# Optimization experiments

Hardware: AMD Instinct MI355X
Metric: run time of the kernel (lower is better)

The kernel has to match this reference:

```python
import jax, jax.numpy as jnp
import numpy as np

VOCAB_SIZE = 62  # string.ascii_letters + string.digits
HIDDEN = 1024
STATE = int(HIDDEN * 4.0)  # state_size_mult=4.0
B, L = 2, 2048


def setup_inputs() -> dict:
    key = jax.random.key(0)
    ks = jax.random.split(key, 6)
    g = lambda k, shape, scale: (jax.random.normal(k, shape, jnp.float32) * scale)
    return {
        "tokens": jax.random.randint(ks[0], (B, L), 0, VOCAB_SIZE),
        "embed_w": g(ks[1], (VOCAB_SIZE, HIDDEN), 1.0),
        "norm_w": jnp.ones((HIDDEN,), jnp.float32),
        "in_w": g(ks[2], (HIDDEN, 4 * STATE), HIDDEN ** -0.5),
        "in_b": jnp.zeros((4 * STATE,), jnp.float32),
        "out_w": g(ks[3], (STATE, HIDDEN), STATE ** -0.5),
        "out_b": jnp.zeros((HIDDEN,), jnp.float32),
        "head_w": g(ks[4], (HIDDEN, VOCAB_SIZE), HIDDEN ** -0.5),
        "head_b": jnp.zeros((VOCAB_SIZE,), jnp.float32),
    }


def _rmsnorm(x, w, eps=1e-6):
    var = jnp.mean(x * x, axis=-1, keepdims=True)
    return x * jax.lax.rsqrt(var + eps) * w


def reference(tokens, embed_w, norm_w, in_w, in_b, out_w, out_b, head_w, head_b):
    # embedding lookup: [B, L, H]
    x = embed_w[tokens]
    res = x
    xn = _rmsnorm(x, norm_w)
    # single fused projection to (x_inner, a, b, c), each [B, L, STATE]
    proj = xn @ in_w + in_b
    xg, a_l, b_l, c_l = jnp.split(proj, 4, axis=-1)
    a = jax.nn.sigmoid(a_l)            # forget gate in (0,1)
    bx = jax.nn.sigmoid(b_l) * xg      # input contribution b_t * x_t
    # linear recurrence h_t = a_t * h_{t-1} + b_t * x_t via associative scan
    def comb(e1, e2):
        a1, h1 = e1
        a2, h2 = e2
        return a1 * a2, a2 * h1 + h2
    _, h = jax.lax.associative_scan(comb, (a, bx), axis=1)
    y = jax.nn.sigmoid(c_l) * h        # output gate c_t * h_t
    out = y @ out_w + out_b + res      # project back to hidden + residual
    return out @ head_w + head_b       # vocab logits [B, L, 62]
```

## Files before the change

kernel.cpp:

```cpp
#include <hip/hip_runtime.h>
#include <math.h>

#define HID   1024
#define STT   4096
#define MTOK  4096
#define LSEQ  2048
#define NCHUNK 64
#define CHUNK  32
#define VOCAB  62

typedef __attribute__((ext_vector_type(8))) short short8v;
typedef __attribute__((ext_vector_type(4))) float float4v;

typedef const __attribute__((address_space(1))) void* gptr_t;
typedef __attribute__((address_space(3))) void* lptr_t;

__device__ __forceinline__ float sigmoidf_(float x) {
    return 1.0f / (1.0f + __expf(-x));
}
__device__ __forceinline__ unsigned short f2bf(float f) {
    unsigned int u = __float_as_uint(f);
    unsigned int r = (u + 0x7fffu + ((u >> 16) & 1u)) >> 16;
    return (unsigned short)r;
}
__device__ __forceinline__ float bf2f(unsigned short b) {
    return __uint_as_float(((unsigned int)b) << 16);
}

__global__ __launch_bounds__(256) void cast_transpose_kernel(
    const float* __restrict__ src, unsigned short* __restrict__ dst, int R, int C)
{
    __shared__ float tile[32][33];
    int c0 = blockIdx.x * 32, r0 = blockIdx.y * 32;
    int t = threadIdx.x;
    int r = t >> 3, c4 = (t & 7) << 2;
    float4 v = *(const float4*)(src + (size_t)(r0 + r) * C + c0 + c4);
    tile[r][c4 + 0] = v.x; tile[r][c4 + 1] = v.y;
    tile[r][c4 + 2] = v.z; tile[r][c4 + 3] = v.w;
    __syncthreads();
    int oc = t >> 3;
    int orr = (t & 7) << 2;
    ushort4 o;
    o.x = f2bf(tile[orr + 0][oc]); o.y = f2bf(tile[orr + 1][oc]);
    o.z = f2bf(tile[orr + 2][oc]); o.w = f2bf(tile[orr + 3][oc]);
    *(ushort4*)(dst + (size_t)(c0 + oc) * R + r0 + orr) = o;
}

__global__ __launch_bounds__(256) void embed_norm_kernel(
    const int* __restrict__ tokens, const float* __restrict__ embed_w,
    const float* __restrict__ norm_w, unsigned short* __restrict__ xn)
{
    int m = blockIdx.x;
    int t = threadIdx.x;
    int tok = tokens[m];
    float4 x = ((const float4*)(embed_w + (size_t)tok * HID))[t];
    float ss = x.x * x.x + x.y * x.y + x.z * x.z + x.w * x.w;
    for (int off = 32; off > 0; off >>= 1) ss += __shfl_down(ss, off);
    __shared__ float wsum[4];
    if ((t & 63) == 0) wsum[t >> 6] = ss;
    __syncthreads();
    float tot = wsum[0] + wsum[1] + wsum[2] + wsum[3];
    float scale = rsqrtf(tot / (float)HID + 1e-6f);
    float4 w4 = ((const float4*)norm_w)[t];
    ushort4 o;
    o.x = f2bf(x.x * scale * w4.x); o.y = f2bf(x.y * scale * w4.y);
    o.z = f2bf(x.z * scale * w4.z); o.w = f2bf(x.w * scale * w4.w);
    *(ushort4*)(xn + (size_t)m * HID + (t << 2)) = o;
}

__global__ __launch_bounds__(256) void w2t_kernel(
    const float* __restrict__ out_w, const float* __restrict__ head_w,
    unsigned short* __restrict__ W2T)
{
    __shared__ float red[4][4][64];
    int tid = threadIdx.x;
    int jc = tid >> 6, n = tid & 63;
    int k0 = blockIdx.x * 4;
    bool act = n < VOCAB;
    float a[4] = {0.f, 0.f, 0.f, 0.f};
    int j0 = jc * 256;
    const float* w0 = out_w + (size_t)(k0 + 0) * HID;
    const float* w1 = out_w + (size_t)(k0 + 1) * HID;
    const float* w2 = out_w + (size_t)(k0 + 2) * HID;
    const float* w3 = out_w + (size_t)(k0 + 3) * HID;
    #pragma unroll 4
    for (int j = j0; j < j0 + 256; j++) {
        float h = act ? head_w[(size_t)j * VOCAB + n] : 0.f;
        a[0] = fmaf(w0[j], h, a[0]);
        a[1] = fmaf(w1[j], h, a[1]);
        a[2] = fmaf(w2[j], h, a[2]);
        a[3] = fmaf(w3[j], h, a[3]);
    }
    #pragma unroll
    for (int i = 0; i < 4; i++) red[jc][i][n] = a[i];
    __syncthreads();
    if (jc == 0) {
        #pragma unroll
        for (int i = 0; i < 4; i++) {
            float s = red[0][i][n] + red[1][i][n] + red[2][i][n] + red[3][i][n];
            W2T[(size_t)n * STT + k0 + i] = f2bf(s);
        }
    }
}

__global__ __launch_bounds__(256) void ehead_kernel(
    const float* __restrict__ embed_w, const float* __restrict__ out_b,
    const float* __restrict__ head_w, const float* __restrict__ head_b,
    float* __restrict__ E_head)
{
    __shared__ float part[4][64];
    int t = blockIdx.x;
    int n = threadIdx.x & 63, jc = threadIdx.x >> 6;
    const float* src = (t < VOCAB) ? (embed_w + (size_t)t * HID) : out_b;
    float acc = 0.f;
    if (n < VOCAB) {
        int j0 = jc * 256;
        #pragma unroll 4
        for (int j = j0; j < j0 + 256; j++)
            acc = fmaf(src[j], head_w[(size_t)j * VOCAB + n], acc);
    }
    part[jc][n] = acc;
    __syncthreads();
    if (threadIdx.x < 64) {
        float s = part[0][n] + part[1][n] + part[2][n] + part[3][n];
        if (t == VOCAB && n < VOCAB) s += head_b[n];
        E_head[t * 64 + n] = s;
    }
}

__global__ __launch_bounds__(512, 2) void gemm_in_mfma(
    const unsigned short* __restrict__ A, const unsigned short* __restrict__ B,
    const float* __restrict__ bias,
    unsigned short* __restrict__ a_out, unsigned short* __restrict__ bx_out,
    unsigned short* __restrict__ c_out)
{
    extern __shared__ unsigned short lds[];
    int tid = threadIdx.x;
    int wid = tid >> 6, lane = tid & 63;
    int wg = blockIdx.x;
    int xcd = wg & 7, loc = wg >> 3;
    int by = ((xcd >> 1) << 2) + (loc & 3);
    int bx = ((xcd & 1) << 5) + (loc >> 2);
    int m0 = by * 256, s0 = bx * 64;
    int wm = wid >> 2, wn = wid & 3;
    int lr = lane & 15, lk = lane >> 4;

    int cb0 = wid * 64, cb1 = 512 + wid * 64;
    int p0 = cb0 + lane, p1 = cb1 + lane;
    int row0 = p0 >> 2, ks0 = (p0 & 3) ^ ((row0 >> 1) & 3);
    int row1 = p1 >> 2, ks1 = (p1 & 3) ^ ((row1 >> 1) & 3);
    int arow0 = m0 + row0, arow1 = m0 + row1;
    int brow0 = ((row0 >> 6) << 12) + s0 + (row0 & 63);
    int brow1 = ((row1 >> 6) << 12) + s0 + (row1 & 63);

#define SHALF(grow0, grow1, b, which, kt, kk) do {                               \
    unsigned short* _d = lds + (b) * 32768 + (which) * 16384 + (kk) * 8192;      \
    __builtin_amdgcn_global_load_lds(                                            \
        (gptr_t)(const void*)(((which) ? B : A) + (size_t)(grow0) * 1024 +       \
                              (kt) * 64 + (kk) * 32 + ks0 * 8),                  \
        (lptr_t)(void*)(_d + (size_t)cb0 * 8), 16, 0, 0);                        \
    __builtin_amdgcn_global_load_lds(                                            \
        (gptr_t)(const void*)(((which) ? B : A) + (size_t)(grow1) * 1024 +       \
                              (kt) * 64 + (kk) * 32 + ks1 * 8),                  \
        (lptr_t)(void*)(_d + (size_t)cb1 * 8), 16, 0, 0);                        \
} while (0)

    int ksw = lk ^ ((lr >> 1) & 3);

#define RD_A(b, kk, mf) \
    (*(const short8v*)&lds[(b) * 32768 + (kk) * 8192 + \
        (((wm * 128 + (mf) * 16 + lr) << 2) + ksw) * 8])
#define RD_B(b, kk, nf) \
    (*(const short8v*)&lds[(b) * 32768 + 16384 + (kk) * 8192 + \
        ((((nf) * 64 + wn * 16 + lr) << 2) + ksw) * 8])

#define MFMA8x2(AF, B0, B1, n0i, n1i) do {                                       \
    __builtin_amdgcn_s_setprio(1);                                               \
    _Pragma("unroll")                                                            \
    for (int mf = 0; mf < 8; mf++) {                                             \
        acc[mf][n0i] = __builtin_amdgcn_mfma_f32_16x16x32_bf16(                  \
            (AF)[mf], (B0), acc[mf][n0i], 0, 0, 0);                              \
        acc[mf][n1i] = __builtin_amdgcn_mfma_f32_16x16x32_bf16(                  \
            (AF)[mf], (B1), acc[mf][n1i], 0, 0, 0);                              \
    }                                                                            \
    __builtin_amdgcn_s_setprio(0);                                               \
} while (0)

#define BAR_IN()  do { __builtin_amdgcn_s_barrier();                              \
    asm volatile("s_waitcnt lgkmcnt(0)" ::: "memory");                           \
    __builtin_amdgcn_sched_barrier(0); } while (0)
#define BAR_OUT() do { asm volatile("" ::: "memory");                             \
    __builtin_amdgcn_s_barrier(); } while (0)

    float4v acc[8][4];
    float4v z = {0.f, 0.f, 0.f, 0.f};
    #pragma unroll
    for (int i = 0; i < 8; i++)
        #pragma unroll
        for (int j = 0; j < 4; j++) acc[i][j] = z;

    SHALF(arow0, arow1, 0, 0, 0, 0); SHALF(brow0, brow1, 0, 1, 0, 0);
    SHALF(arow0, arow1, 0, 0, 0, 1); SHALF(brow0, brow1, 0, 1, 0, 1);
    asm volatile("s_waitcnt vmcnt(0)" ::: "memory");
    __builtin_amdgcn_s_barrier();

    short8v af[8], bf0, bf1;

    for (int kt = 0; kt < 16; ++kt) {
        int cur = kt & 1, nxt = cur ^ 1;
        int ktn = kt < 15 ? kt + 1 : 15;
        #pragma unroll
        for (int mf = 0; mf < 8; mf++) af[mf] = RD_A(cur, 0, mf);
        bf0 = RD_B(cur, 0, 0); bf1 = RD_B(cur, 0, 1);
        asm volatile("s_waitcnt vmcnt(4)" ::: "memory");
        SHALF(arow0, arow1, nxt, 0, ktn, 0);
        BAR_IN();
        MFMA8x2(af, bf0, bf1, 0, 1);
        BAR_OUT();
        bf0 = RD_B(cur, 0, 2); bf1 = RD_B(cur, 0, 3);
        SHALF(brow0, brow1, nxt, 1, ktn, 0);
        BAR_IN();
        MFMA8x2(af, bf0, bf1, 2, 3);
        BAR_OUT();
        #pragma unroll
        for (int mf = 0; mf < 8; mf++) af[mf] = RD_A(cur, 1, mf);
        bf0 = RD_B(cur, 1, 0); bf1 = RD_B(cur, 1, 1);
        asm volatile("s_waitcnt vmcnt(4)" ::: "memory");
        SHALF(arow0, arow1, nxt, 0, ktn, 1);
        BAR_IN();
        MFMA8x2(af, bf0, bf1, 0, 1);
        BAR_OUT();
        bf0 = RD_B(cur, 1, 2); bf1 = RD_B(cur, 1, 3);
        SHALF(brow0, brow1, nxt, 1, ktn, 1);
        BAR_IN();
        MFMA8x2(af, bf0, bf1, 2, 3);
        BAR_OUT();
    }

    int s = s0 + wn * 16 + lr;
    float b_xg = bias[s];
    float b_a  = bias[4096 + s];
    float b_b  = bias[8192 + s];
    float b_c  = bias[12288 + s];
    int rbase = lk << 2;
    #pragma unroll
    for (int mf = 0; mf < 8; mf++)
        #pragma unroll
        for (int q = 0; q < 4; q++) {
            int m = m0 + wm * 128 + mf * 16 + rbase + q;
            size_t idx = (size_t)m * STT + s;
            float xg = acc[mf][0][q] + b_xg;
            float a  = sigmoidf_(acc[mf][1][q] + b_a);
            float bxv = sigmoidf_(acc[mf][2][q] + b_b) * xg;
            float c  = sigmoidf_(acc[mf][3][q] + b_c);
            a_out[idx]  = f2bf(a);
            bx_out[idx] = f2bf(bxv);
            c_out[idx]  = f2bf(c);
        }
#undef SHALF
#undef RD_A
#undef RD_B
#undef MFMA8x2
#undef BAR_IN
#undef BAR_OUT
}

__global__ __launch_bounds__(256, 3) void logits_gemm(
    const unsigned short* __restrict__ Y, const unsigned short* __restrict__ W2T,
    float* __restrict__ part)
{
    extern __shared__ unsigned short lds[];
    int tid = threadIdx.x;
    int wid = tid >> 6, lane = tid & 63;
    int wg = blockIdx.x;
    int m0 = (wg & 31) * 128;
    int slice = wg >> 5;
    int ks0 = slice * 512;
    int wm = wid >> 1, wn = wid & 1;
    int lr = lane & 15, lk = lane >> 4;

    auto stage = [&](int b, int kt) {
        unsigned short* As = lds + b * 6144;
        unsigned short* Bs = As + 4096;
        #pragma unroll
        for (int i = 0; i < 2; i++) {
            int cb = i * 256 + wid * 64;
            int p = cb + lane;
            int row = p >> 2;
            int ks = (p & 3) ^ ((row >> 1) & 3);
            __builtin_amdgcn_global_load_lds(
                (gptr_t)(const void*)(Y + (size_t)(m0 + row) * STT + kt + ks * 8),
                (lptr_t)(void*)(As + (size_t)cb * 8), 16, 0, 0);
        }
        {
            int cb = wid * 64;
            int p = cb + lane;
            int row = p >> 2;
            int ks = (p & 3) ^ ((row >> 1) & 3);
            __builtin_amdgcn_global_load_lds(
                (gptr_t)(const void*)(W2T + (size_t)row * STT + kt + ks * 8),
                (lptr_t)(void*)(Bs + (size_t)cb * 8), 16, 0, 0);
        }
    };

    float4v acc[4][2];
    float4v z = {0.f, 0.f, 0.f, 0.f};
    #pragma unroll
    for (int i = 0; i < 4; i++) { acc[i][0] = z; acc[i][1] = z; }

    const int nt = 16;
    stage(0, ks0); stage(1, ks0 + 32);

    int ksw = lk ^ ((lr >> 1) & 3);

    for (int t = 0; t < nt; ++t) {
        if (t + 2 < nt) stage((t + 2) % 3, ks0 + (t + 2) * 32);
        if (t + 2 < nt)      asm volatile("s_waitcnt vmcnt(6)" ::: "memory");
        else if (t + 1 < nt) asm volatile("s_waitcnt vmcnt(3)" ::: "memory");
        else                 asm volatile("s_waitcnt vmcnt(0)" ::: "memory");
        __builtin_amdgcn_s_barrier();
        asm volatile("" ::: "memory");
        const unsigned short* As = lds + (t % 3) * 6144;
        const unsigned short* Bs = As + 4096;
        short8v af[4], bfr[2];
        #pragma unroll
        for (int f = 0; f < 4; f++)
            af[f] = *(const short8v*)&As[(((wm * 64 + f * 16 + lr) << 2) + ksw) * 8];
        #pragma unroll
        for (int g = 0; g < 2; g++)
            bfr[g] = *(const short8v*)&Bs[(((wn * 32 + g * 16 + lr) << 2) + ksw) * 8];
        __builtin_amdgcn_s_setprio(1);
        #pragma unroll
        for (int f = 0; f < 4; f++)
            #pragma unroll
            for (int g = 0; g < 2; g++)
                acc[f][g] = __builtin_amdgcn_mfma_f32_16x16x32_bf16(
                    af[f], bfr[g], acc[f][g], 0, 0, 0);
        __builtin_amdgcn_s_setprio(0);
        asm volatile("" ::: "memory");
        __builtin_amdgcn_s_barrier();
    }

    float* pb = part + (size_t)slice * MTOK * 64;
    int rbase = lk << 2;
    #pragma unroll
    for (int f = 0; f < 4; f++)
        #pragma unroll
        for (int g = 0; g < 2; g++) {
            int n = wn * 32 + g * 16 + lr;
            #pragma unroll
            for (int q = 0; q < 4; q++) {
                int m = m0 + wm * 64 + f * 16 + rbase + q;
                pb[(size_t)m * 64 + n] = acc[f][g][q];
            }
        }
}

__global__ __launch_bounds__(64) void logits_reduce(
    const float* __restrict__ part, const float* __restrict__ E_head,
    const int* __restrict__ tokens, float* __restrict__ logits)
{
    int m = blockIdx.x;
    int n = threadIdx.x;
    if (n >= VOCAB) return;
    int tok = tokens[m];
    float s = E_head[tok * 64 + n] + E_head[VOCAB * 64 + n];
    #pragma unroll
    for (int sl = 0; sl < 8; sl++)
        s += part[(size_t)sl * MTOK * 64 + (size_t)m * 64 + n];
    logits[(size_t)m * VOCAB + n] = s;
}

__global__ __launch_bounds__(256) void scan_phase1(
    const unsigned short* __restrict__ a_buf, const unsigned short* __restrict__ bx_buf,
    float* __restrict__ chunkA, float* __restrict__ chunkH)
{
    int bid = blockIdx.x;
    int sg = bid & 3, q = (bid >> 2) & 63, b = bid >> 8;
    int s0 = sg * 1024 + threadIdx.x * 4;
    size_t base = (size_t)(b * LSEQ + q * CHUNK) * STT + s0;
    const unsigned short* ap = a_buf + base;
    const unsigned short* bp = bx_buf + base;
    float Aa[4] = {1.f, 1.f, 1.f, 1.f}, Hh[4] = {0.f, 0.f, 0.f, 0.f};
    for (int t = 0; t < CHUNK; t++) {
        ushort4 Av = *(const ushort4*)ap;
        ushort4 Bv = *(const ushort4*)bp;
        const unsigned short* avp = (const unsigned short*)&Av;
        const unsigned short* bvp = (const unsigned short*)&Bv;
        #pragma unroll
        for (int j = 0; j < 4; j++) {
            float a = bf2f(avp[j]);
            Hh[j] = fmaf(a, Hh[j], bf2f(bvp[j]));
            Aa[j] *= a;
        }
        ap += STT; bp += STT;
    }
    #pragma unroll
    for (int j = 0; j < 4; j++) {
        int ch = b * STT + s0 + j;
        chunkA[ch * NCHUNK + q] = Aa[j];
        chunkH[ch * NCHUNK + q] = Hh[j];
    }
}

__global__ __launch_bounds__(256) void scan_phase2(
    const float* __restrict__ chunkA, const float* __restrict__ chunkH,
    float* __restrict__ carry)
{
    int ch = blockIdx.x * 256 + threadIdx.x;
    float c = 0.f;
    for (int q = 0; q < NCHUNK; q++) {
        carry[ch * NCHUNK + q] = c;
        c = fmaf(chunkA[ch * NCHUNK + q], c, chunkH[ch * NCHUNK + q]);
    }
}

__global__ __launch_bounds__(256) void scan_phase3(
    const unsigned short* __restrict__ a_buf, const unsigned short* __restrict__ bx_buf,
    const unsigned short* __restrict__ c_buf, const float* __restrict__ carry,
    unsigned short* __restrict__ y)
{
    int bid = blockIdx.x;
    int sg = bid & 3, q = (bid >> 2) & 63, b = bid >> 8;
    int s0 = sg * 1024 + threadIdx.x * 4;
    float h[4];
    #pragma unroll
    for (int j = 0; j < 4; j++)
        h[j] = carry[(b * STT + s0 + j) * NCHUNK + q];
    size_t base = (size_t)(b * LSEQ + q * CHUNK) * STT + s0;
    const unsigned short* ap = a_buf + base;
    const unsigned short* bp = bx_buf + base;
    const unsigned short* cp = c_buf + base;
    unsigned short* yp = y + base;
    for (int t = 0; t < CHUNK; t++) {
        ushort4 Av = *(const ushort4*)ap;
        ushort4 Bv = *(const ushort4*)bp;
        ushort4 Cv = *(const ushort4*)cp;
        const unsigned short* avp = (const unsigned short*)&Av;
        const unsigned short* bvp = (const unsigned short*)&Bv;
        const unsigned short* cvp = (const unsigned short*)&Cv;
        ushort4 o;
        unsigned short* op = (unsigned short*)&o;
        #pragma unroll
        for (int j = 0; j < 4; j++) {
            h[j] = fmaf(bf2f(avp[j]), h[j], bf2f(bvp[j]));
            op[j] = f2bf(bf2f(cvp[j]) * h[j]);
        }
        *(ushort4*)yp = o;
        ap += STT; bp += STT; cp += STT; yp += STT;
    }
}

extern "C" void kernel_launch(void* const* d_in, const int* in_sizes, int n_in,
                              void* d_out, int out_size, void* d_ws, size_t ws_size,
                              hipStream_t stream) {
    const int*   tokens  = (const int*)d_in[0];
    const float* embed_w = (const float*)d_in[1];
    const float* norm_w  = (const float*)d_in[2];
    const float* in_w    = (const float*)d_in[3];
    const float* in_b    = (const float*)d_in[4];
    const float* out_w   = (const float*)d_in[5];
    const float* out_b   = (const float*)d_in[6];
    const float* head_w  = (const float*)d_in[7];
    const float* head_b  = (const float*)d_in[8];
    float* logits = (float*)d_out;

    char* w = (char*)d_ws;
    unsigned short* a_buf  = (unsigned short*)w;
    unsigned short* bx_buf = (unsigned short*)(w + 33554432);
    unsigned short* c_buf  = (unsigned short*)(w + 67108864);
    unsigned short* W2T    = (unsigned short*)(w + 100663296);
    float*          E_head = (float*)(w + 101711872);
    float*          part   = (float*)(w + 102760448);
    unsigned short* y      = (unsigned short*)(w + 134217728);
    unsigned short* in_wT  = (unsigned short*)(w + 167772160);
    unsigned short* xn     = (unsigned short*)(w + 201326592);
    float* chunkA = (float*)(w + 209715200);
    float* chunkH = chunkA + 8192 * NCHUNK;
    float* carry  = chunkH + 8192 * NCHUNK;

    hipLaunchKernelGGL(cast_transpose_kernel, dim3(16384 / 32, 1024 / 32), dim3(256), 0, stream,
                       in_w, in_wT, 1024, 16384);
    hipLaunchKernelGGL(embed_norm_kernel, dim3(MTOK), dim3(256), 0, stream,
                       tokens, embed_w, norm_w, xn);
    hipLaunchKernelGGL(w2t_kernel, dim3(1024), dim3(256), 0, stream,
                       out_w, head_w, W2T);
    hipLaunchKernelGGL(ehead_kernel, dim3(VOCAB + 1), dim3(256), 0, stream,
                       embed_w, out_b, head_w, head_b, E_head);
    hipLaunchKernelGGL(gemm_in_mfma, dim3(1024), dim3(512), 131072, stream,
                       xn, in_wT, in_b, a_buf, bx_buf, c_buf);
    hipLaunchKernelGGL(scan_phase1, dim3(512), dim3(256), 0, stream,
                       a_buf, bx_buf, chunkA, chunkH);
    hipLaunchKernelGGL(scan_phase2, dim3(32), dim3(256), 0, stream,
                       chunkA, chunkH, carry);
    hipLaunchKernelGGL(scan_phase3, dim3(512), dim3(256), 0, stream,
                       a_buf, bx_buf, c_buf, carry, y);
    hipLaunchKernelGGL(logits_gemm, dim3(256), dim3(256), 36864, stream,
                       y, W2T, part);
    hipLaunchKernelGGL(logits_reduce, dim3(MTOK), dim3(64), 0, stream,
                       part, E_head, tokens, logits);
}
```

Baseline: 291.2 us.

## Shrink input GEMM tiles to single-buffered 128x128 blocks and merge prep kernels

The fused input projection GEMM moves from 256x256 output tiles with 512 threads and double-buffered 128KB LDS to 128x128 tiles (32 state columns times four gates) with 256 threads, a 16KB static LDS tile and a simple load-wait-compute loop over k-steps of 32. The aim is higher occupancy and more workgroups to spread across CUs. In exchange it gives up load/compute overlap, lowers MFMA work per LDS byte and adds a barrier every k-step. Separately, the W2T and E_head precompute kernels are merged into one launch to cut launch overhead.

```diff
diff --git a/kernel.cpp b/kernel.cpp
--- a/kernel.cpp
+++ b/kernel.cpp
@@ -68,201 +68,160 @@
     *(ushort4*)(xn + (size_t)m * HID + (t << 2)) = o;
 }
 
-__global__ __launch_bounds__(256) void w2t_kernel(
+__global__ __launch_bounds__(256) void prep_kernel(
     const float* __restrict__ out_w, const float* __restrict__ head_w,
-    unsigned short* __restrict__ W2T)
+    const float* __restrict__ embed_w, const float* __restrict__ out_b,
+    const float* __restrict__ head_b,
+    unsigned short* __restrict__ W2T, float* __restrict__ E_head)
 {
     __shared__ float red[4][4][64];
     int tid = threadIdx.x;
     int jc = tid >> 6, n = tid & 63;
-    int k0 = blockIdx.x * 4;
     bool act = n < VOCAB;
-    float a[4] = {0.f, 0.f, 0.f, 0.f};
-    int j0 = jc * 256;
-    const float* w0 = out_w + (size_t)(k0 + 0) * HID;
-    const float* w1 = out_w + (size_t)(k0 + 1) * HID;
-    const float* w2 = out_w + (size_t)(k0 + 2) * HID;
-    const float* w3 = out_w + (size_t)(k0 + 3) * HID;
-    #pragma unroll 4
-    for (int j = j0; j < j0 + 256; j++) {
-        float h = act ? head_w[(size_t)j * VOCAB + n] : 0.f;
-        a[0] = fmaf(w0[j], h, a[0]);
-        a[1] = fmaf(w1[j], h, a[1]);
-        a[2] = fmaf(w2[j], h, a[2]);
-        a[3] = fmaf(w3[j], h, a[3]);
-    }
-    #pragma unroll
-    for (int i = 0; i < 4; i++) red[jc][i][n] = a[i];
-    __syncthreads();
-    if (jc == 0) {
-        #pragma unroll
-        for (int i = 0; i < 4; i++) {
-            float s = red[0][i][n] + red[1][i][n] + red[2][i][n] + red[3][i][n];
-            W2T[(size_t)n * STT + k0 + i] = f2bf(s);
-        }
-    }
-}
-
-__global__ __launch_bounds__(256) void ehead_kernel(
-    const float* __restrict__ embed_w, const float* __restrict__ out_b,
-    const float* __restrict__ head_w, const float* __restrict__ head_b,
-    float* __restrict__ E_head)
-{
-    __shared__ float part[4][64];
-    int t = blockIdx.x;
-    int n = threadIdx.x & 63, jc = threadIdx.x >> 6;
-    const float* src = (t < VOCAB) ? (embed_w + (size_t)t * HID) : out_b;
-    float acc = 0.f;
-    if (n < VOCAB) {
+    if (blockIdx.x < 1024) {
+        int k0 = blockIdx.x * 4;
+        float a[4] = {0.f, 0.f, 0.f, 0.f};
         int j0 = jc * 256;
+        const float* w0 = out_w + (size_t)(k0 + 0) * HID;
+        const float* w1 = out_w + (size_t)(k0 + 1) * HID;
+        const float* w2 = out_w + (size_t)(k0 + 2) * HID;
+        const float* w3 = out_w + (size_t)(k0 + 3) * HID;
         #pragma unroll 4
-        for (int j = j0; j < j0 + 256; j++)
-            acc = fmaf(src[j], head_w[(size_t)j * VOCAB + n], acc);
-    }
-    part[jc][n] = acc;
-    __syncthreads();
-    if (threadIdx.x < 64) {
-        float s = part[0][n] + part[1][n] + part[2][n] + part[3][n];
-        if (t == VOCAB && n < VOCAB) s += head_b[n];
-        E_head[t * 64 + n] = s;
-    }
-}
-
-__global__ __launch_bounds__(512, 2) void gemm_in_mfma(
+        for (int j = j0; j < j0 + 256; j++) {
+            float h = act ? head_w[(size_t)j * VOCAB + n] : 0.f;
+            a[0] = fmaf(w0[j], h, a[0]);
+            a[1] = fmaf(w1[j], h, a[1]);
+            a[2] = fmaf(w2[j], h, a[2]);
+            a[3] = fmaf(w3[j], h, a[3]);
+        }
+        #pragma unroll
+        for (int i = 0; i < 4; i++) red[jc][i][n] = a[i];
+        __syncthreads();
+        if (jc == 0) {
+            #pragma unroll
+            for (int i = 0; i < 4; i++) {
+                float s = red[0][i][n] + red[1][i][n] + red[2][i][n] + red[3][i][n];
+                W2T[(size_t)n * STT + k0 + i] = f2bf(s);
+            }
+        }
+    } else {
+        int t = blockIdx.x - 1024;
+        const float* src = (t < VOCAB) ? (embed_w + (size_t)t * HID) : out_b;
+        float acc = 0.f;
+        if (act) {
+            int j0 = jc * 256;
+            #pragma unroll 4
+            for (int j = j0; j < j0 + 256; j++)
+                acc = fmaf(src[j], head_w[(size_t)j * VOCAB + n], acc);
+        }
+        red[jc][0][n] = acc;
+        __syncthreads();
+        if (tid < 64) {
+            float s = red[0][0][n] + red[1][0][n] + red[2][0][n] + red[3][0][n];
+            if (t == VOCAB && act) s += head_b[n];
+            E_head[t * 64 + n] = s;
+        }
+    }
+}
+
+__global__ __launch_bounds__(256) void gemm_in_mfma(
     const unsigned short* __restrict__ A, const unsigned short* __restrict__ B,
     const float* __restrict__ bias,
     unsigned short* __restrict__ a_out, unsigned short* __restrict__ bx_out,
     unsigned short* __restrict__ c_out)
 {
-    extern __shared__ unsigned short lds[];
+    __shared__ __align__(16) unsigned short lds[8192];
     int tid = threadIdx.x;
     int wid = tid >> 6, lane = tid & 63;
     int wg = blockIdx.x;
     int xcd = wg & 7, loc = wg >> 3;
-    int by = ((xcd >> 1) << 2) + (loc & 3);
-    int bx = ((xcd & 1) << 5) + (loc >> 2);
-    int m0 = by * 256, s0 = bx * 64;
-    int wm = wid >> 2, wn = wid & 3;
+    int by = (xcd >> 2) * 16 + (loc & 15);
+    int slab = (xcd & 3) * 32 + (loc >> 4);
+    int m0 = by * 128, s0 = slab * 32;
     int lr = lane & 15, lk = lane >> 4;
 
-    int cb0 = wid * 64, cb1 = 512 + wid * 64;
+    int cb0 = wid * 64, cb1 = 256 + wid * 64;
     int p0 = cb0 + lane, p1 = cb1 + lane;
-    int row0 = p0 >> 2, ks0 = (p0 & 3) ^ ((row0 >> 1) & 3);
-    int row1 = p1 >> 2, ks1 = (p1 & 3) ^ ((row1 >> 1) & 3);
-    int arow0 = m0 + row0, arow1 = m0 + row1;
-    int brow0 = ((row0 >> 6) << 12) + s0 + (row0 & 63);
-    int brow1 = ((row1 >> 6) << 12) + s0 + (row1 & 63);
-
-#define SHALF(grow0, grow1, b, which, kt, kk) do {                               \
-    unsigned short* _d = lds + (b) * 32768 + (which) * 16384 + (kk) * 8192;      \
+    int r0 = p0 >> 2, k0s = (p0 & 3) ^ ((r0 >> 1) & 3);
+    int r1 = p1 >> 2, k1s = (p1 & 3) ^ ((r1 >> 1) & 3);
+    int arow0 = m0 + r0, arow1 = m0 + r1;
+    int bcol0 = ((r0 >> 5) << 12) + s0 + (r0 & 31);
+    int bcol1 = ((r1 >> 5) << 12) + s0 + (r1 & 31);
+
+#define STAGE(kt) do {                                                           \
     __builtin_amdgcn_global_load_lds(                                            \
-        (gptr_t)(const void*)(((which) ? B : A) + (size_t)(grow0) * 1024 +       \
-                              (kt) * 64 + (kk) * 32 + ks0 * 8),                  \
-        (lptr_t)(void*)(_d + (size_t)cb0 * 8), 16, 0, 0);                        \
+        (gptr_t)(const void*)(A + (size_t)arow0 * 1024 + (kt) * 32 + k0s * 8),   \
+        (lptr_t)(void*)(lds + cb0 * 8), 16, 0, 0);                               \
     __builtin_amdgcn_global_load_lds(                                            \
-        (gptr_t)(const void*)(((which) ? B : A) + (size_t)(grow1) * 1024 +       \
-                              (kt) * 64 + (kk) * 32 + ks1 * 8),                  \
-        (lptr_t)(void*)(_d + (size_t)cb1 * 8), 16, 0, 0);                        \
+        (gptr_t)(const void*)(A + (size_t)arow1 * 1024 + (kt) * 32 + k1s * 8),   \
+        (lptr_t)(void*)(lds + cb1 * 8), 16, 0, 0);                               \
+    __builtin_amdgcn_global_load_lds(                                            \
+        (gptr_t)(const void*)(B + (size_t)bcol0 * 1024 + (kt) * 32 + k0s * 8),   \
+        (lptr_t)(void*)(lds + 4096 + cb0 * 8), 16, 0, 0);                        \
+    __builtin_amdgcn_global_load_lds(                                            \
+        (gptr_t)(const void*)(B + (size_t)bcol1 * 1024 + (kt) * 32 + k1s * 8),   \
+        (lptr_t)(void*)(lds + 4096 + cb1 * 8), 16, 0, 0);                        \
 } while (0)
 
     int ksw = lk ^ ((lr >> 1) & 3);
 
-#define RD_A(b, kk, mf) \
-    (*(const short8v*)&lds[(b) * 32768 + (kk) * 8192 + \
-        (((wm * 128 + (mf) * 16 + lr) << 2) + ksw) * 8])
-#define RD_B(b, kk, nf) \
-    (*(const short8v*)&lds[(b) * 32768 + 16384 + (kk) * 8192 + \
-        ((((nf) * 64 + wn * 16 + lr) << 2) + ksw) * 8])
-
-#define MFMA8x2(AF, B0, B1, n0i, n1i) do {                                       \
-    __builtin_amdgcn_s_setprio(1);                                               \
-    _Pragma("unroll")                                                            \
-    for (int mf = 0; mf < 8; mf++) {                                             \
-        acc[mf][n0i] = __builtin_amdgcn_mfma_f32_16x16x32_bf16(                  \
-            (AF)[mf], (B0), acc[mf][n0i], 0, 0, 0);                              \
-        acc[mf][n1i] = __builtin_amdgcn_mfma_f32_16x16x32_bf16(                  \
-            (AF)[mf], (B1), acc[mf][n1i], 0, 0, 0);                              \
-    }                                                                            \
-    __builtin_amdgcn_s_setprio(0);                                               \
-} while (0)
-
-#define BAR_IN()  do { __builtin_amdgcn_s_barrier();                              \
-    asm volatile("s_waitcnt lgkmcnt(0)" ::: "memory");                           \
-    __builtin_amdgcn_sched_barrier(0); } while (0)
-#define BAR_OUT() do { asm volatile("" ::: "memory");                             \
-    __builtin_amdgcn_s_barrier(); } while (0)
-
-    float4v acc[8][4];
+    float4v acc[2][8];
     float4v z = {0.f, 0.f, 0.f, 0.f};
     #pragma unroll
-    for (int i = 0; i < 8; i++)
-        #pragma unroll
-        for (int j = 0; j < 4; j++) acc[i][j] = z;
-
-    SHALF(arow0, arow1, 0, 0, 0, 0); SHALF(brow0, brow1, 0, 1, 0, 0);
-    SHALF(arow0, arow1, 0, 0, 0, 1); SHALF(brow0, brow1, 0, 1, 0, 1);
-    asm volatile("s_waitcnt vmcnt(0)" ::: "memory");
-    __builtin_amdgcn_s_barrier();
-
-    short8v af[8], bf0, bf1;
-
-    for (int kt = 0; kt < 16; ++kt) {
-        int cur = kt & 1, nxt = cur ^ 1;
-        int ktn = kt < 15 ? kt + 1 : 15;
-        #pragma unroll
-        for (int mf = 0; mf < 8; mf++) af[mf] = RD_A(cur, 0, mf);
-        bf0 = RD_B(cur, 0, 0); bf1 = RD_B(cur, 0, 1);
-        asm volatile("s_waitcnt vmcnt(4)" ::: "memory");
-        SHALF(arow0, arow1, nxt, 0, ktn, 0);
-        BAR_IN();
-        MFMA8x2(af, bf0, bf1, 0, 1);
-        BAR_OUT();
-        bf0 = RD_B(cur, 0, 2); bf1 = RD_B(cur, 0, 3);
-        SHALF(brow0, brow1, nxt, 1, ktn, 0);
-        BAR_IN();
-        MFMA8x2(af, bf0, bf1, 2, 3);
-        BAR_OUT();
-        #pragma unroll
-        for (int mf = 0; mf < 8; mf++) af[mf] = RD_A(cur, 1, mf);
-        bf0 = RD_B(cur, 1, 0); bf1 = RD_B(cur, 1, 1);
-        asm volatile("s_waitcnt vmcnt(4)" ::: "memory");
-        SHALF(arow0, arow1, nxt, 0, ktn, 1);
-        BAR_IN();
-        MFMA8x2(af, bf0, bf1, 0, 1);
-        BAR_OUT();
-        bf0 = RD_B(cur, 1, 2); bf1 = RD_B(cur, 1, 3);
-        SHALF(brow0, brow1, nxt, 1, ktn, 1);
-        BAR_IN();
-        MFMA8x2(af, bf0, bf1, 2, 3);
-        BAR_OUT();
-    }
-
-    int s = s0 + wn * 16 + lr;
-    float b_xg = bias[s];
-    float b_a  = bias[4096 + s];
-    float b_b  = bias[8192 + s];
-    float b_c  = bias[12288 + s];
+    for (int i = 0; i < 2; i++)
+        #pragma unroll
+        for (int j = 0; j < 8; j++) acc[i][j] = z;
+
+    for (int kt = 0; kt < 32; ++kt) {
+        STAGE(kt);
+        asm volatile("s_waitcnt vmcnt(0)" ::: "memory");
+        __builtin_amdgcn_s_barrier();
+        short8v af0 = *(const short8v*)&lds[(((wid * 32 + lr) << 2) + ksw) * 8];
+        short8v af1 = *(const short8v*)&lds[(((wid * 32 + 16 + lr) << 2) + ksw) * 8];
+        short8v bf[8];
+        #pragma unroll
+        for (int nf = 0; nf < 8; nf++)
+            bf[nf] = *(const short8v*)&lds[4096 + (((nf * 16 + lr) << 2) + ksw) * 8];
+        __builtin_amdgcn_s_setprio(1);
+        #pragma unroll
+        for (int nf = 0; nf < 8; nf++) {
+            acc[0][nf] = __builtin_amdgcn_mfma_f32_16x16x32_bf16(af0, bf[nf], acc[0][nf], 0, 0, 0);
+            acc[1][nf] = __builtin_amdgcn_mfma_f32_16x16x32_bf16(af1, bf[nf], acc[1][nf], 0, 0, 0);
+        }
+        __builtin_amdgcn_s_setprio(0);
+        asm volatile("" ::: "memory");
+        __builtin_amdgcn_s_barrier();
+    }
+#undef STAGE
+
+    float b_xg[2], b_a[2], b_b[2], b_c[2];
+    #pragma unroll
+    for (int h = 0; h < 2; h++) {
+        int s = s0 + h * 16 + lr;
+        b_xg[h] = bias[s];
+        b_a[h]  = bias[4096 + s];
+        b_b[h]  = bias[8192 + s];
+        b_c[h]  = bias[12288 + s];
+    }
     int rbase = lk << 2;
     #pragma unroll
-    for (int mf = 0; mf < 8; mf++)
+    for (int mf = 0; mf < 2; mf++)
         #pragma unroll
         for (int q = 0; q < 4; q++) {
-            int m = m0 + wm * 128 + mf * 16 + rbase + q;
-            size_t idx = (size_t)m * STT + s;
-            float xg = acc[mf][0][q] + b_xg;
-            float a  = sigmoidf_(acc[mf][1][q] + b_a);
-            float bxv = sigmoidf_(acc[mf][2][q] + b_b) * xg;
-            float c  = sigmoidf_(acc[mf][3][q] + b_c);
-            a_out[idx]  = f2bf(a);
-            bx_out[idx] = f2bf(bxv);
-            c_out[idx]  = f2bf(c);
-        }
-#undef SHALF
-#undef RD_A
-#undef RD_B
-#undef MFMA8x2
-#undef BAR_IN
-#undef BAR_OUT
+            int m = m0 + wid * 32 + mf * 16 + rbase + q;
+            #pragma unroll
+            for (int h = 0; h < 2; h++) {
+                int s = s0 + h * 16 + lr;
+                size_t idx = (size_t)m * STT + s;
+                float xg = acc[mf][0 + h][q] + b_xg[h];
+                float a  = sigmoidf_(acc[mf][2 + h][q] + b_a[h]);
+                float bxv = sigmoidf_(acc[mf][4 + h][q] + b_b[h]) * xg;
+                float c  = sigmoidf_(acc[mf][6 + h][q] + b_c[h]);
+                a_out[idx]  = f2bf(a);
+                bx_out[idx] = f2bf(bxv);
+                c_out[idx]  = f2bf(c);
+            }
+        }
 }
 
 __global__ __launch_bounds__(256, 3) void logits_gemm(
@@ -483,11 +442,9 @@
                        in_w, in_wT, 1024, 16384);
     hipLaunchKernelGGL(embed_norm_kernel, dim3(MTOK), dim3(256), 0, stream,
                        tokens, embed_w, norm_w, xn);
-    hipLaunchKernelGGL(w2t_kernel, dim3(1024), dim3(256), 0, stream,
-                       out_w, head_w, W2T);
-    hipLaunchKernelGGL(ehead_kernel, dim3(VOCAB + 1), dim3(256), 0, stream,
-                       embed_w, out_b, head_w, head_b, E_head);
-    hipLaunchKernelGGL(gemm_in_mfma, dim3(1024), dim3(512), 131072, stream,
+    hipLaunchKernelGGL(prep_kernel, dim3(1024 + VOCAB + 1), dim3(256), 0, stream,
+                       out_w, head_w, embed_w, out_b, head_b, W2T, E_head);
+    hipLaunchKernelGGL(gemm_in_mfma, dim3(4096), dim3(256), 0, stream,
                        xn, in_wT, in_b, a_buf, bx_buf, c_buf);
     hipLaunchKernelGGL(scan_phase1, dim3(512), dim3(256), 0, stream,
                        a_buf, bx_buf, chunkA, chunkH);
```

New measurement: 309.4 us. 6.3% more time.
